# Optimization experiments

Measured on AMD Instinct MI355X. Metric: run time of the kernel, lower is better.

## Reference

```python
import jax, jax.numpy as jnp
import numpy as np

B, N, D = 2, 2048, 512
H, HD = 8, 64
R = 64  # graph_radius
SCALE = HD ** -0.5
LN_EPS = 1e-5


def _ln(x, g, b):
    m = jnp.mean(x, axis=-1, keepdims=True)
    v = jnp.mean((x - m) ** 2, axis=-1, keepdims=True)
    return (x - m) * jax.lax.rsqrt(v + LN_EPS) * g + b


def setup_inputs() -> dict:
    key = jax.random.key(0)
    ks = jax.random.split(key, 8)
    w = lambda k, shape: (jax.random.normal(k, shape, jnp.float32) * 0.02)
    return {
        "nodes": jax.random.normal(ks[0], (B, N, D), jnp.float32),
        "ln1_g": jnp.ones((D,), jnp.float32), "ln1_b": jnp.zeros((D,), jnp.float32),
        "qkv_w": w(ks[1], (D, 3 * D)), "qkv_b": jnp.zeros((3 * D,), jnp.float32),
        "proj_w": w(ks[2], (D, D)), "proj_b": jnp.zeros((D,), jnp.float32),
        "rep_scale": jnp.ones((H,), jnp.float32),
        "rel_bias": w(ks[3], (2 * N - 1, H)),
        "ln2_g": jnp.ones((D,), jnp.float32), "ln2_b": jnp.zeros((D,), jnp.float32),
        "mlp_w1": w(ks[4], (D, 2 * D)), "mlp_b1": jnp.zeros((2 * D,), jnp.float32),
        "mlp_w2": w(ks[5], (2 * D, D)), "mlp_b2": jnp.zeros((D,), jnp.float32),
    }


def reference(nodes, ln1_g, ln1_b, qkv_w, qkv_b, proj_w, proj_b, rep_scale,
              rel_bias, ln2_g, ln2_b, mlp_w1, mlp_b1, mlp_w2, mlp_b2):
    b, n, d = nodes.shape
    x = _ln(nodes, ln1_g, ln1_b)                       # [B,N,D]
    qkv = (x @ qkv_w + qkv_b).reshape(b, n, 3, H, HD)
    qkv = jnp.transpose(qkv, (2, 0, 3, 1, 4))          # [3,B,H,N,HD]
    q, k, v = qkv[0], qkv[1], qkv[2]
    logits = jnp.einsum('bhnd,bhmd->bhnm', q, k) * SCALE
    # representation correlation (F.normalize with eps=1e-12)
    rep = x / jnp.maximum(jnp.linalg.norm(x, axis=-1, keepdims=True), 1e-12)
    corr = jnp.einsum('bnd,bmd->bnm', rep, rep)        # [B,N,N]
    logits = logits + corr[:, None] * rep_scale[None, :, None, None]
    pos = jnp.arange(n)
    relidx = pos[:, None] - pos[None, :]               # [N,N]
    bias = rel_bias[relidx + n - 1]                    # [N,N,H]
    logits = logits + jnp.transpose(bias, (2, 0, 1))[None]
    mask = jnp.abs(relidx) <= R
    logits = jnp.where(mask[None, None], logits, -jnp.inf)
    attn = jax.nn.softmax(logits, axis=-1)
    upd = jnp.einsum('bhnm,bhmd->bnhd', attn, v).reshape(b, n, d)
    nodes = nodes + (upd @ proj_w + proj_b)
    y = _ln(nodes, ln2_g, ln2_b)
    h = jax.nn.gelu(y @ mlp_w1 + mlp_b1, approximate=False)
    return nodes + (h @ mlp_w2 + mlp_b2)
```

## Files before the change

kernel.cpp:

```cpp
#include <hip/hip_runtime.h>
#include <math.h>

typedef __bf16 bf16;
typedef __bf16 bf16x4 __attribute__((ext_vector_type(4)));
typedef __bf16 bf16x8 __attribute__((ext_vector_type(8)));
typedef float floatx4 __attribute__((ext_vector_type(4)));

#define BB 2
#define NN 2048
#define DD 512
#define HH 8
#define HD 64
#define RR 64
#define D3 1536
#define NEG_BIG (-1e30f)
#define TQ 32
#define TBAND 160
#define VW 200

#define GL2LDS16(g, l)                                                        \
    __builtin_amdgcn_global_load_lds(                                         \
        (const __attribute__((address_space(1))) void*)(const void*)(g),      \
        (__attribute__((address_space(3))) void*)(void*)(l), 16, 0, 0)

__global__ __launch_bounds__(256) void cvt_t_kernel(
    const float* __restrict__ W, bf16* __restrict__ Wt, int K, int N) {
    __shared__ bf16 Ts[64][72];
    const int tid = threadIdx.x;
    const int n0 = blockIdx.x * 64, k0 = blockIdx.y * 64;
    #pragma unroll
    for (int i = 0; i < 4; i++) {
        int r = (tid >> 4) + i * 16;
        int c = (tid & 15) * 4;
        floatx4 v = *(const floatx4*)(W + (size_t)(k0 + r) * N + n0 + c);
        #pragma unroll
        for (int e = 0; e < 4; e++) Ts[r][c + e] = (bf16)v[e];
    }
    __syncthreads();
    #pragma unroll
    for (int i = 0; i < 4; i++) {
        int n = (tid >> 4) + i * 16;
        int k = (tid & 15) * 4;
        bf16x4 o;
        #pragma unroll
        for (int e = 0; e < 4; e++) o[e] = Ts[k + e][n];
        *(bf16x4*)(Wt + (size_t)(n0 + n) * K + k0 + k) = o;
    }
}

__device__ inline float block_reduce_sum256(float v, float* sbuf) {
    const int tid = threadIdx.x;
    #pragma unroll
    for (int o = 32; o > 0; o >>= 1) v += __shfl_xor(v, o, 64);
    __syncthreads();
    if ((tid & 63) == 0) sbuf[tid >> 6] = v;
    __syncthreads();
    return sbuf[0] + sbuf[1] + sbuf[2] + sbuf[3];
}

template <bool WANT_INV>
__global__ __launch_bounds__(256) void ln_kernel(
    const float* __restrict__ in, const float* __restrict__ gw,
    const float* __restrict__ bw, bf16* __restrict__ out,
    float* __restrict__ invnorm) {
    __shared__ float sbuf[4];
    const int row = blockIdx.x, tid = threadIdx.x;
    const int i0 = tid * 2;
    const float* ip = in + (size_t)row * DD;
    float v0 = ip[i0], v1 = ip[i0 + 1];
    float mean = block_reduce_sum256(v0 + v1, sbuf) * (1.f / DD);
    float d0 = v0 - mean, d1 = v1 - mean;
    float var = block_reduce_sum256(d0 * d0 + d1 * d1, sbuf) * (1.f / DD);
    float rs = rsqrtf(var + 1e-5f);
    float x0 = d0 * rs * gw[i0] + bw[i0];
    float x1 = d1 * rs * gw[i0 + 1] + bw[i0 + 1];
    out[(size_t)row * DD + i0] = (bf16)x0;
    out[(size_t)row * DD + i0 + 1] = (bf16)x1;
    if (WANT_INV) {
        float s2 = block_reduce_sum256(x0 * x0 + x1 * x1, sbuf);
        if (tid == 0) invnorm[row] = 1.f / fmaxf(sqrtf(s2), 1e-12f);
    }
}

template <int MODE, int BND>
__global__ __launch_bounds__(256) void gemm_bt(
    const bf16* __restrict__ A, const bf16* __restrict__ Bt,
    const float* __restrict__ bias, const float* __restrict__ resid,
    void* __restrict__ out, int M, int N, int K) {
    __shared__ __align__(16) bf16 As[128 * 32];
    __shared__ __align__(16) bf16 Bs[BND * 32];
    const int tid = threadIdx.x;
    const int w = tid >> 6, lane = tid & 63;
    const int rowBase = blockIdx.y * 128, colBase = blockIdx.x * BND;
    const int lr = lane & 15, lq = lane >> 4;
    constexpr int MI = (BND == 128) ? 4 : 2;
    const int wm = (BND == 128) ? (w >> 1) * 64 : w * 32;
    const int wn = (BND == 128) ? (w & 1) * 64 : 0;

    floatx4 acc[MI][4];
    #pragma unroll
    for (int i = 0; i < MI; i++)
        #pragma unroll
        for (int j = 0; j < 4; j++) acc[i][j] = (floatx4){0.f, 0.f, 0.f, 0.f};

    for (int k0 = 0; k0 < K; k0 += 32) {
        __syncthreads();
        #pragma unroll
        for (int i = 0; i < 2; i++) {
            int s = (w * 2 + i) * 64 + lane;
            GL2LDS16(A + (size_t)(rowBase + (s >> 2)) * K + k0 + (s & 3) * 8,
                     As + s * 8);
        }
        #pragma unroll
        for (int i = 0; i < BND / 64; i++) {
            int s = (w * (BND / 64) + i) * 64 + lane;
            GL2LDS16(Bt + (size_t)(colBase + (s >> 2)) * K + k0 + (s & 3) * 8,
                     Bs + s * 8);
        }
        __syncthreads();

        bf16x8 af[MI], bfr[4];
        #pragma unroll
        for (int i = 0; i < MI; i++)
            af[i] = *(bf16x8*)&As[(wm + i * 16 + lr) * 32 + lq * 8];
        #pragma unroll
        for (int j = 0; j < 4; j++)
            bfr[j] = *(bf16x8*)&Bs[(wn + j * 16 + lr) * 32 + lq * 8];
        #pragma unroll
        for (int i = 0; i < MI; i++)
            #pragma unroll
            for (int j = 0; j < 4; j++)
                acc[i][j] = __builtin_amdgcn_mfma_f32_16x16x32_bf16(
                    af[i], bfr[j], acc[i][j], 0, 0, 0);
    }

    #pragma unroll
    for (int i = 0; i < MI; i++) {
        #pragma unroll
        for (int j = 0; j < 4; j++) {
            #pragma unroll
            for (int r = 0; r < 4; r++) {
                int row = rowBase + wm + i * 16 + lq * 4 + r;
                int col = colBase + wn + j * 16 + lr;
                size_t idx = (size_t)row * N + col;
                float v = acc[i][j][r] + bias[col];
                if (MODE == 0) {
                    ((bf16*)out)[idx] = (bf16)v;
                } else if (MODE == 1) {
                    ((float*)out)[idx] = v + resid[idx];
                } else if (MODE == 2) {
                    float g = 0.5f * v * (1.f + erff(v * 0.70710678118654752f));
                    ((bf16*)out)[idx] = (bf16)g;
                } else {
                    ((float*)out)[idx] = v + resid[idx];
                }
            }
        }
    }
}

__global__ __launch_bounds__(256) void attn_kernel(
    const bf16* __restrict__ x, const float* __restrict__ invnorm,
    const bf16* __restrict__ qkv, const float* __restrict__ rep_scale,
    const float* __restrict__ rel_bias, bf16* __restrict__ upd) {
    __shared__ __align__(16) bf16 Qs[TQ][72];
    __shared__ __align__(16) bf16 Ks[TBAND][72];
    __shared__ __align__(16) bf16 Vt[64 * VW];
    __shared__ __align__(16) bf16 Ps[TQ][168];
    __shared__ float relb[4][192];
    __shared__ float invb[TBAND];
    __shared__ float rmax2[TQ][2];
    __shared__ float rsum2[TQ][2];

    const int tid = threadIdx.x;
    const int bid = blockIdx.x;
    const int b = bid & 1;
    const int h0 = ((bid >> 1) & 1) * 4;
    const int n0 = (bid >> 2) * TQ;
    const int bN = b * NN;

    const int w = tid >> 6, lane = tid & 63;
    const int lr = lane & 15, lq = lane >> 4;
    const int rowHalf = (w >> 1) * 16;
    const int colBase = (w & 1) * 80;
    const int c2 = (w & 1) * 32;

    if (tid < TBAND) {
        int mc = min(max(n0 - RR + tid, 0), NN - 1);
        invb[tid] = invnorm[bN + mc];
    }
    for (int idx = tid; idx < 4 * 191; idx += 256) {
        int hh = idx / 191, dh = idx - hh * 191;
        relb[hh][dh] = rel_bias[(size_t)(dh + (NN - 1 - 95)) * HH + h0 + hh];
    }

    floatx4 cacc[5];
    #pragma unroll
    for (int t = 0; t < 5; t++) cacc[t] = (floatx4){0.f, 0.f, 0.f, 0.f};

    for (int c = 0; c < 8; c++) {
        __syncthreads();
        #pragma unroll
        for (int i = 0; i < 5; i++) {
            int s = i * 256 + tid;
            int j = s >> 3, seg = s & 7;
            int mc = min(max(n0 - RR + j, 0), NN - 1);
            *(bf16x8*)&Ks[j][seg * 8] =
                *(const bf16x8*)(x + (size_t)(bN + mc) * DD + c * 64 + seg * 8);
        }
        __syncthreads();
        #pragma unroll
        for (int kb = 0; kb < 2; kb++) {
            bf16x8 a = *(bf16x8*)&Ks[64 + rowHalf + lr][kb * 32 + lq * 8];
            #pragma unroll
            for (int t = 0; t < 5; t++) {
                bf16x8 bb = *(bf16x8*)&Ks[colBase + t * 16 + lr][kb * 32 + lq * 8];
                cacc[t] = __builtin_amdgcn_mfma_f32_16x16x32_bf16(a, bb, cacc[t], 0, 0, 0);
            }
        }
    }
    __syncthreads();

    float corrv[5][4];
    {
        float invq[4];
        #pragma unroll
        for (int r = 0; r < 4; r++) invq[r] = invb[64 + rowHalf + lq * 4 + r];
        #pragma unroll
        for (int t = 0; t < 5; t++) {
            float invk = invb[colBase + t * 16 + lr];
            #pragma unroll
            for (int r = 0; r < 4; r++) corrv[t][r] = cacc[t][r] * invq[r] * invk;
        }
    }

    for (int h = h0; h < h0 + 4; h++) {
        {
            int row = tid >> 3, seg = tid & 7;
            *(bf16x8*)&Qs[row][seg * 8] =
                *(const bf16x8*)(qkv + (size_t)(bN + n0 + row) * D3 + h * HD + seg * 8);
        }
        #pragma unroll
        for (int i = 0; i < 5; i++) {
            int s = i * 256 + tid;
            int j = s >> 3, seg = s & 7;
            int mc = min(max(n0 - RR + j, 0), NN - 1);
            *(bf16x8*)&Ks[j][seg * 8] =
                *(const bf16x8*)(qkv + (size_t)(bN + mc) * D3 + DD + h * HD + seg * 8);
            bf16x8 v = *(const bf16x8*)(qkv + (size_t)(bN + mc) * D3 + 2 * DD + h * HD + seg * 8);
            #pragma unroll
            for (int e = 0; e < 8; e++) {
                int d = seg * 8 + e;
                int key = (d >> 2) & 7;
                int jsw = (j & 7) | (((j >> 3) ^ key) << 3);
                Vt[d * VW + jsw] = v[e];
            }
        }
        __syncthreads();

        floatx4 sacc[5];
        #pragma unroll
        for (int t = 0; t < 5; t++) sacc[t] = (floatx4){0.f, 0.f, 0.f, 0.f};
        #pragma unroll
        for (int kb = 0; kb < 2; kb++) {
            bf16x8 a = *(bf16x8*)&Qs[rowHalf + lr][kb * 32 + lq * 8];
            #pragma unroll
            for (int t = 0; t < 5; t++) {
                bf16x8 bb = *(bf16x8*)&Ks[colBase + t * 16 + lr][kb * 32 + lq * 8];
                sacc[t] = __builtin_amdgcn_mfma_f32_16x16x32_bf16(a, bb, sacc[t], 0, 0, 0);
            }
        }

        const float srep = rep_scale[h];
        float l[5][4];
        float mx[4] = {NEG_BIG, NEG_BIG, NEG_BIG, NEG_BIG};
        #pragma unroll
        for (int t = 0; t < 5; t++) {
            int j = colBase + t * 16 + lr;
            int m = n0 - RR + j;
            #pragma unroll
            for (int r = 0; r < 4; r++) {
                int qi = rowHalf + lq * 4 + r;
                int relidx = qi + RR - j;
                bool valid = (relidx >= -RR) && (relidx <= RR) && (m >= 0) && (m < NN);
                float lv = sacc[t][r] * 0.125f + corrv[t][r] * srep +
                           relb[h - h0][relidx + 95];
                l[t][r] = valid ? lv : NEG_BIG;
                mx[r] = fmaxf(mx[r], l[t][r]);
            }
        }
        #pragma unroll
        for (int r = 0; r < 4; r++)
            #pragma unroll
            for (int mk = 1; mk <= 8; mk <<= 1)
                mx[r] = fmaxf(mx[r], __shfl_xor(mx[r], mk, 64));
        if (lr == 0) {
            #pragma unroll
            for (int r = 0; r < 4; r++) rmax2[rowHalf + lq * 4 + r][w & 1] = mx[r];
        }
        __syncthreads();

        float rm[4], sm[4];
        #pragma unroll
        for (int r = 0; r < 4; r++) {
            int row = rowHalf + lq * 4 + r;
            rm[r] = fmaxf(rmax2[row][0], rmax2[row][1]);
            sm[r] = 0.f;
        }
        #pragma unroll
        for (int t = 0; t < 5; t++) {
            int j = colBase + t * 16 + lr;
            #pragma unroll
            for (int r = 0; r < 4; r++) {
                float pv = __expf(l[t][r] - rm[r]);
                sm[r] += pv;
                Ps[rowHalf + lq * 4 + r][j] = (bf16)pv;
            }
        }
        #pragma unroll
        for (int r = 0; r < 4; r++)
            #pragma unroll
            for (int mk = 1; mk <= 8; mk <<= 1)
                sm[r] += __shfl_xor(sm[r], mk, 64);
        if (lr == 0) {
            #pragma unroll
            for (int r = 0; r < 4; r++) rsum2[rowHalf + lq * 4 + r][w & 1] = sm[r];
        }
        __syncthreads();

        floatx4 oacc[2] = {(floatx4){0.f, 0.f, 0.f, 0.f}, (floatx4){0.f, 0.f, 0.f, 0.f}};
        #pragma unroll
        for (int kb = 0; kb < 5; kb++) {
            bf16x8 a = *(bf16x8*)&Ps[rowHalf + lr][kb * 32 + lq * 8];
            #pragma unroll
            for (int tt = 0; tt < 2; tt++) {
                int d = c2 + tt * 16 + lr;
                int key = (d >> 2) & 7;
                int jsw = (kb * 32 + lq * 8) ^ (key << 3);
                bf16x8 bb = *(bf16x8*)&Vt[d * VW + jsw];
                oacc[tt] = __builtin_amdgcn_mfma_f32_16x16x32_bf16(a, bb, oacc[tt], 0, 0, 0);
            }
        }
        #pragma unroll
        for (int r = 0; r < 4; r++) {
            int row = rowHalf + lq * 4 + r;
            float rinv = 1.f / (rsum2[row][0] + rsum2[row][1]);
            #pragma unroll
            for (int tt = 0; tt < 2; tt++) {
                upd[(size_t)(bN + n0 + row) * DD + h * HD + c2 + tt * 16 + lr] =
                    (bf16)(oacc[tt][r] * rinv);
            }
        }
        __syncthreads();
    }
}

extern "C" void kernel_launch(void* const* d_in, const int* in_sizes, int n_in,
                              void* d_out, int out_size, void* d_ws,
                              size_t ws_size, hipStream_t stream) {
    const float* nodes  = (const float*)d_in[0];
    const float* ln1_g  = (const float*)d_in[1];
    const float* ln1_b  = (const float*)d_in[2];
    const float* qkv_w  = (const float*)d_in[3];
    const float* qkv_b  = (const float*)d_in[4];
    const float* proj_w = (const float*)d_in[5];
    const float* proj_b = (const float*)d_in[6];
    const float* rep_s  = (const float*)d_in[7];
    const float* rel_b  = (const float*)d_in[8];
    const float* ln2_g  = (const float*)d_in[9];
    const float* ln2_b  = (const float*)d_in[10];
    const float* mlp_w1 = (const float*)d_in[11];
    const float* mlp_b1 = (const float*)d_in[12];
    const float* mlp_w2 = (const float*)d_in[13];
    const float* mlp_b2 = (const float*)d_in[14];

    char* p = (char*)d_ws;
    float* invn = (float*)p;            p += (size_t)1 << 20;
    bf16*  wqt  = (bf16*)p;             p += (size_t)DD * D3 * 2;
    bf16*  wpt  = (bf16*)p;             p += (size_t)DD * DD * 2;
    bf16*  w1t  = (bf16*)p;             p += (size_t)DD * 2 * DD * 2;
    bf16*  w2t  = (bf16*)p;             p += (size_t)2 * DD * DD * 2;
    bf16*  x    = (bf16*)p;             p += (size_t)BB * NN * DD * 2;
    bf16*  qkvb = (bf16*)p;             p += (size_t)BB * NN * D3 * 2;
    float* mid  = (float*)p;            p += (size_t)BB * NN * DD * 4;
    bf16*  y    = x;
    bf16*  hgl  = qkvb;
    bf16*  upd  = (bf16*)d_out;

    const int M = BB * NN;

    cvt_t_kernel<<<dim3(D3 / 64, DD / 64), 256, 0, stream>>>(qkv_w, wqt, DD, D3);
    cvt_t_kernel<<<dim3(DD / 64, DD / 64), 256, 0, stream>>>(proj_w, wpt, DD, DD);
    cvt_t_kernel<<<dim3(2 * DD / 64, DD / 64), 256, 0, stream>>>(mlp_w1, w1t, DD, 2 * DD);
    cvt_t_kernel<<<dim3(DD / 64, 2 * DD / 64), 256, 0, stream>>>(mlp_w2, w2t, 2 * DD, DD);

    ln_kernel<true><<<M, 256, 0, stream>>>(nodes, ln1_g, ln1_b, x, invn);
    gemm_bt<0, 128><<<dim3(D3 / 128, M / 128), 256, 0, stream>>>(
        x, wqt, qkv_b, nullptr, qkvb, M, D3, DD);
    attn_kernel<<<(NN / TQ) * 2 * BB, 256, 0, stream>>>(
        x, invn, qkvb, rep_s, rel_b, upd);
    gemm_bt<1, 64><<<dim3(DD / 64, M / 128), 256, 0, stream>>>(
        upd, wpt, proj_b, nodes, mid, M, DD, DD);
    ln_kernel<false><<<M, 256, 0, stream>>>(mid, ln2_g, ln2_b, y, nullptr);
    gemm_bt<2, 128><<<dim3(2 * DD / 128, M / 128), 256, 0, stream>>>(
        y, w1t, mlp_b1, nullptr, hgl, M, 2 * DD, DD);
    gemm_bt<3, 64><<<dim3(DD / 64, M / 128), 256, 0, stream>>>(
        hgl, w2t, mlp_b2, mid, (float*)d_out, M, DD, 2 * DD);
}
```

Baseline: 204.8 us.

## Double-buffer GEMM LDS tiles with XOR swizzle and uniform 64x64 tiles

```diff
diff --git a/kernel.cpp b/kernel.cpp
--- a/kernel.cpp
+++ b/kernel.cpp
@@ -82,62 +82,76 @@
     }
 }
 
-template <int MODE, int BND>
+template <int MODE>
 __global__ __launch_bounds__(256) void gemm_bt(
     const bf16* __restrict__ A, const bf16* __restrict__ Bt,
     const float* __restrict__ bias, const float* __restrict__ resid,
     void* __restrict__ out, int M, int N, int K) {
-    __shared__ __align__(16) bf16 As[128 * 32];
-    __shared__ __align__(16) bf16 Bs[BND * 32];
+    __shared__ __align__(16) bf16 As[2][64 * 64];
+    __shared__ __align__(16) bf16 Bs[2][64 * 64];
     const int tid = threadIdx.x;
     const int w = tid >> 6, lane = tid & 63;
-    const int rowBase = blockIdx.y * 128, colBase = blockIdx.x * BND;
     const int lr = lane & 15, lq = lane >> 4;
-    constexpr int MI = (BND == 128) ? 4 : 2;
-    const int wm = (BND == 128) ? (w >> 1) * 64 : w * 32;
-    const int wn = (BND == 128) ? (w & 1) * 64 : 0;
-
-    floatx4 acc[MI][4];
-    #pragma unroll
-    for (int i = 0; i < MI; i++)
-        #pragma unroll
-        for (int j = 0; j < 4; j++) acc[i][j] = (floatx4){0.f, 0.f, 0.f, 0.f};
-
-    for (int k0 = 0; k0 < K; k0 += 32) {
-        __syncthreads();
+    const int rowBase = blockIdx.y * 64, colBase = blockIdx.x * 64;
+    const int wm = (w >> 1) * 32, wn = (w & 1) * 32;
+
+    floatx4 acc[2][2];
+    #pragma unroll
+    for (int i = 0; i < 2; i++)
+        #pragma unroll
+        for (int j = 0; j < 2; j++) acc[i][j] = (floatx4){0.f, 0.f, 0.f, 0.f};
+
+    auto stage = [&](int buf, int k0) {
         #pragma unroll
         for (int i = 0; i < 2; i++) {
-            int s = (w * 2 + i) * 64 + lane;
-            GL2LDS16(A + (size_t)(rowBase + (s >> 2)) * K + k0 + (s & 3) * 8,
-                     As + s * 8);
-        }
-        #pragma unroll
-        for (int i = 0; i < BND / 64; i++) {
-            int s = (w * (BND / 64) + i) * 64 + lane;
-            GL2LDS16(Bt + (size_t)(colBase + (s >> 2)) * K + k0 + (s & 3) * 8,
-                     Bs + s * 8);
-        }
-        __syncthreads();
-
-        bf16x8 af[MI], bfr[4];
-        #pragma unroll
-        for (int i = 0; i < MI; i++)
-            af[i] = *(bf16x8*)&As[(wm + i * 16 + lr) * 32 + lq * 8];
-        #pragma unroll
-        for (int j = 0; j < 4; j++)
-            bfr[j] = *(bf16x8*)&Bs[(wn + j * 16 + lr) * 32 + lq * 8];
-        #pragma unroll
-        for (int i = 0; i < MI; i++)
-            #pragma unroll
-            for (int j = 0; j < 4; j++)
-                acc[i][j] = __builtin_amdgcn_mfma_f32_16x16x32_bf16(
-                    af[i], bfr[j], acc[i][j], 0, 0, 0);
-    }
-
-    #pragma unroll
-    for (int i = 0; i < MI; i++) {
-        #pragma unroll
-        for (int j = 0; j < 4; j++) {
+            int g = i * 256 + tid;
+            int row = g >> 3, k8 = (g & 7) ^ (row & 7);
+            GL2LDS16(A + (size_t)(rowBase + row) * K + k0 + k8 * 8,
+                     &As[buf][g * 8]);
+        }
+        #pragma unroll
+        for (int i = 0; i < 2; i++) {
+            int g = i * 256 + tid;
+            int row = g >> 3, k8 = (g & 7) ^ (row & 7);
+            GL2LDS16(Bt + (size_t)(colBase + row) * K + k0 + k8 * 8,
+                     &Bs[buf][g * 8]);
+        }
+    };
+
+    const int nsteps = K >> 6;
+    stage(0, 0);
+    for (int s = 0; s < nsteps; s++) {
+        __syncthreads();
+        if (s + 1 < nsteps) stage((s + 1) & 1, (s + 1) * 64);
+        const int buf = s & 1;
+        #pragma unroll
+        for (int kb = 0; kb < 2; kb++) {
+            bf16x8 af[2], bfr[2];
+            #pragma unroll
+            for (int i = 0; i < 2; i++) {
+                int row = wm + i * 16 + lr;
+                int g = row * 8 + ((kb * 4 + lq) ^ (row & 7));
+                af[i] = *(bf16x8*)&As[buf][g * 8];
+            }
+            #pragma unroll
+            for (int j = 0; j < 2; j++) {
+                int row = wn + j * 16 + lr;
+                int g = row * 8 + ((kb * 4 + lq) ^ (row & 7));
+                bfr[j] = *(bf16x8*)&Bs[buf][g * 8];
+            }
+            #pragma unroll
+            for (int i = 0; i < 2; i++)
+                #pragma unroll
+                for (int j = 0; j < 2; j++)
+                    acc[i][j] = __builtin_amdgcn_mfma_f32_16x16x32_bf16(
+                        af[i], bfr[j], acc[i][j], 0, 0, 0);
+        }
+    }
+
+    #pragma unroll
+    for (int i = 0; i < 2; i++) {
+        #pragma unroll
+        for (int j = 0; j < 2; j++) {
             #pragma unroll
             for (int r = 0; r < 4; r++) {
                 int row = rowBase + wm + i * 16 + lq * 4 + r;
@@ -395,15 +409,15 @@
     cvt_t_kernel<<<dim3(DD / 64, 2 * DD / 64), 256, 0, stream>>>(mlp_w2, w2t, 2 * DD, DD);
 
     ln_kernel<true><<<M, 256, 0, stream>>>(nodes, ln1_g, ln1_b, x, invn);
-    gemm_bt<0, 128><<<dim3(D3 / 128, M / 128), 256, 0, stream>>>(
+    gemm_bt<0><<<dim3(D3 / 64, M / 64), 256, 0, stream>>>(
         x, wqt, qkv_b, nullptr, qkvb, M, D3, DD);
     attn_kernel<<<(NN / TQ) * 2 * BB, 256, 0, stream>>>(
         x, invn, qkvb, rep_s, rel_b, upd);
-    gemm_bt<1, 64><<<dim3(DD / 64, M / 128), 256, 0, stream>>>(
+    gemm_bt<1><<<dim3(DD / 64, M / 64), 256, 0, stream>>>(
         upd, wpt, proj_b, nodes, mid, M, DD, DD);
     ln_kernel<false><<<M, 256, 0, stream>>>(mid, ln2_g, ln2_b, y, nullptr);
-    gemm_bt<2, 128><<<dim3(2 * DD / 128, M / 128), 256, 0, stream>>>(
+    gemm_bt<2><<<dim3(2 * DD / 64, M / 64), 256, 0, stream>>>(
         y, w1t, mlp_b1, nullptr, hgl, M, 2 * DD, DD);
-    gemm_bt<3, 64><<<dim3(DD / 64, M / 128), 256, 0, stream>>>(
+    gemm_bt<3><<<dim3(DD / 64, M / 64), 256, 0, stream>>>(
         hgl, w2t, mlp_b2, mid, (float*)d_out, M, DD, 2 * DD);
 }
```

New measurement: 182.8 us. 10.7% less time.
